# Kernel optimization log

Measured on AMD Instinct MI355X. Metric: run time of the kernel, lower is better.

## Reference

```python
import jax, jax.numpy as jnp
import numpy as np

S, B, V, E, H = 64, 32, 32000, 512, 1024


def gru_cell(x, h, Wih, Whh, bih, bhh):
    # PyTorch GRU cell math. x: [B, in], h: [B, H]
    gi = x @ Wih.T + bih          # [B, 3H]
    gh = h @ Whh.T + bhh          # [B, 3H]
    ir, iz, inn = jnp.split(gi, 3, axis=-1)
    hr, hz, hn = jnp.split(gh, 3, axis=-1)
    r = jax.nn.sigmoid(ir + hr)
    z = jax.nn.sigmoid(iz + hz)
    n = jnp.tanh(inn + r * hn)
    return (1.0 - z) * n + z * h


def run_gru(xs, h0, Wih, Whh, bih, bhh):
    def step(h, x):
        h = gru_cell(x, h, Wih, Whh, bih, bhh)
        return h, h
    _, hs = jax.lax.scan(step, h0, xs)
    return hs  # [S, B, H]


def setup_inputs():
    key = jax.random.key(0)
    ks = jax.random.split(key, 24)
    n = lambda k, shp, s=0.05: (jax.random.normal(k, shp, jnp.float32) * s)
    inp = {
        "input_seq": jax.random.randint(ks[0], (S, B), 0, V),
        "target_seq": jax.random.randint(ks[1], (S, B), 0, V),
        "emb": n(ks[2], (V, E)),
        # bidirectional encoder GRU (forward / backward directions)
        "enc_Wih_f": n(ks[3], (3 * H, E)), "enc_Whh_f": n(ks[4], (3 * H, H)),
        "enc_bih_f": n(ks[5], (3 * H,)),  "enc_bhh_f": n(ks[6], (3 * H,)),
        "enc_Wih_b": n(ks[7], (3 * H, E)), "enc_Whh_b": n(ks[8], (3 * H, H)),
        "enc_bih_b": n(ks[9], (3 * H,)),  "enc_bhh_b": n(ks[10], (3 * H,)),
        "encoder_init": n(ks[11], (2, H), 0.1),
        # decoder GRU: input = token(E) + glimpse(2H) + last_output(E)
        "dec_Wih": n(ks[12], (3 * H, 2 * E + 2 * H)), "dec_Whh": n(ks[13], (3 * H, H)),
        "dec_bih": n(ks[14], (3 * H,)), "dec_bhh": n(ks[15], (3 * H,)),
        "dec_init_h": n(ks[16], (H,), 0.1),
        "dec_init_out": n(ks[17], (E,), 0.1),
        "attn_W1": n(ks[18], (H, 3 * H)),  # Linear(3H -> H, bias=False)
        "attn_W2": n(ks[19], (1, H)),      # Linear(H -> 1, bias=False)
        "out_W": n(ks[20], (V, H)), "out_b": n(ks[21], (V,)),
    }
    return inp


def reference(input_seq, target_seq, emb,
              enc_Wih_f, enc_Whh_f, enc_bih_f, enc_bhh_f,
              enc_Wih_b, enc_Whh_b, enc_bih_b, enc_bhh_b, encoder_init,
              dec_Wih, dec_Whh, dec_bih, dec_bhh, dec_init_h, dec_init_out,
              attn_W1, attn_W2, out_W, out_b):
    x = emb[input_seq]            # [S, B, E]
    tgt = emb[target_seq]         # [S, B, E]
    bsz = x.shape[1]

    # bidirectional encoder
    h0f = jnp.broadcast_to(encoder_init[0], (bsz, H))
    h0b = jnp.broadcast_to(encoder_init[1], (bsz, H))
    fwd = run_gru(x, h0f, enc_Wih_f, enc_Whh_f, enc_bih_f, enc_bhh_f)
    bwd = run_gru(x[::-1], h0b, enc_Wih_b, enc_Whh_b, enc_bih_b, enc_bhh_b)[::-1]
    enc = jnp.concatenate([fwd, bwd], axis=-1)  # [S, B, 2H]

    def step(carry, inp_t):
        h, last_out = carry                      # [B,H], [B,E]
        tok, tg = inp_t                          # [B,E], [B,E]
        hexp = jnp.broadcast_to(h[None], (S, bsz, H))
        a = jnp.concatenate([enc, hexp], axis=-1)            # [S, B, 3H]
        scores = jnp.tanh(a @ attn_W1.T) @ attn_W2.T          # [S, B, 1]
        # NOTE: original uses nn.Softmax(dim=1) on [S,B,1] -> softmax over BATCH dim
        w = jax.nn.softmax(scores, axis=1)
        glimpse = (enc * w).sum(axis=0)                       # [B, 2H]
        dec_in = jnp.concatenate([tok, glimpse, last_out], axis=-1)
        h = gru_cell(dec_in, h, dec_Wih, dec_Whh, dec_bih, dec_bhh)
        probs = jax.nn.softmax(h @ out_W.T + out_b, axis=1)   # [B, V]
        return (h, tg), probs

    h0 = jnp.broadcast_to(dec_init_h, (bsz, H))
    o0 = jnp.broadcast_to(dec_init_out, (bsz, E))
    _, outs = jax.lax.scan(step, (h0, o0), (x, tgt))
    return outs  # [S, B, V]
```

## Files before the change

### kernel.cpp

```cpp
#include <hip/hip_runtime.h>
#include <hip/hip_bf16.h>

#define S_ 64
#define B_ 32
#define V_ 32000
#define E_ 512
#define H_ 1024
#define H3_ 3072

typedef __hip_bfloat16 bf16;
typedef __attribute__((ext_vector_type(8))) short s8v;
typedef __attribute__((ext_vector_type(4))) float f4;
typedef unsigned long long ull;

__device__ __forceinline__ float b2f(bf16 x){ return __bfloat162float(x); }
__device__ __forceinline__ bf16  f2b(float x){ return __float2bfloat16(x); }
__device__ __forceinline__ float bfu2f(unsigned short u){
  union { unsigned u; float f; } c; c.u = ((unsigned)u) << 16; return c.f;
}
#define MFMA16(a,b,c) __builtin_amdgcn_mfma_f32_16x16x32_bf16((a),(b),(c),0,0,0)

__device__ __forceinline__ float fsigmoid(float x){ return 1.f/(1.f + __expf(-x)); }
__device__ __forceinline__ float ftanh(float x){ float e2 = __expf(2.f*x); return 1.f - 2.f/(e2 + 1.f); }

__global__ __launch_bounds__(256) void cast_bf16_k(const float* __restrict__ s, bf16* __restrict__ d, int n8){
  int stride = gridDim.x*256;
  for (int i = blockIdx.x*256 + threadIdx.x; i < n8; i += stride){
    f4 a = *((const f4*)s + (size_t)i*2);
    f4 b = *((const f4*)s + (size_t)i*2 + 1);
    union { s8v v; bf16 h[8]; } o;
    #pragma unroll
    for (int k=0;k<4;k++){ o.h[k]=f2b(a[k]); o.h[4+k]=f2b(b[k]); }
    *((s8v*)d + i) = o.v;
  }
}
__global__ __launch_bounds__(256) void cast2_k(const float* __restrict__ s0, const float* __restrict__ s1,
                                               bf16* __restrict__ d0, bf16* __restrict__ d1, int n8){
  const float* s = blockIdx.y ? s1 : s0;
  bf16* d = blockIdx.y ? d1 : d0;
  int stride = gridDim.x*256;
  for (int i = blockIdx.x*256 + threadIdx.x; i < n8; i += stride){
    f4 a = *((const f4*)s + (size_t)i*2);
    f4 b = *((const f4*)s + (size_t)i*2 + 1);
    union { s8v v; bf16 h[8]; } o;
    #pragma unroll
    for (int k=0;k<4;k++){ o.h[k]=f2b(a[k]); o.h[4+k]=f2b(b[k]); }
    *((s8v*)d + i) = o.v;
  }
}
__global__ __launch_bounds__(256) void cast4_k(const float* __restrict__ s0, const float* __restrict__ s1,
                                               const float* __restrict__ s2, const float* __restrict__ s3,
                                               bf16* __restrict__ d0, bf16* __restrict__ d1,
                                               bf16* __restrict__ d2, bf16* __restrict__ d3, int n8){
  const float* s = (blockIdx.y==0)?s0:(blockIdx.y==1)?s1:(blockIdx.y==2)?s2:s3;
  bf16* d = (blockIdx.y==0)?d0:(blockIdx.y==1)?d1:(blockIdx.y==2)?d2:d3;
  int stride = gridDim.x*256;
  for (int i = blockIdx.x*256 + threadIdx.x; i < n8; i += stride){
    f4 a = *((const f4*)s + (size_t)i*2);
    f4 b = *((const f4*)s + (size_t)i*2 + 1);
    union { s8v v; bf16 h[8]; } o;
    #pragma unroll
    for (int k=0;k<4;k++){ o.h[k]=f2b(a[k]); o.h[4+k]=f2b(b[k]); }
    *((s8v*)d + i) = o.v;
  }
}
__global__ __launch_bounds__(256) void gather2_k(const float* __restrict__ emb,
                                                 const int* __restrict__ iseq, const int* __restrict__ tseq,
                                                 const float* __restrict__ o0,
                                                 bf16* __restrict__ dx, bf16* __restrict__ dlo){
  int i = blockIdx.x*256 + threadIdx.x;
  int row = i >> 6, e8 = i & 63;
  const float* src;
  bf16* d;
  if (blockIdx.y == 0){
    src = emb + (size_t)iseq[row]*E_;
    d = dx;
  } else {
    int t = row >> 5, b = row & 31;
    src = (t == 0) ? o0 : (emb + (size_t)tseq[(t-1)*B_ + b]*E_);
    d = dlo;
  }
  f4 a = *((const f4*)src + e8*2);
  f4 b = *((const f4*)src + e8*2 + 1);
  union { s8v v; bf16 h[8]; } o;
  #pragma unroll
  for (int k=0;k<4;k++){ o.h[k]=f2b(a[k]); o.h[4+k]=f2b(b[k]); }
  *((s8v*)d + i) = o.v;
}

template<int WB16, int ACC>
__global__ __launch_bounds__(256) void gemm_bt(const bf16* __restrict__ A, int lda,
                                               const bf16* __restrict__ B, int ldb,
                                               const float* __restrict__ bias,
                                               void* __restrict__ Cp, int ldc, int K)
{
  __shared__ bf16 a_sm[128][40];
  __shared__ bf16 b_sm[128][40];
  const int tid = threadIdx.x;
  const int m0 = blockIdx.y*128, n0 = blockIdx.x*128;
  const int w = tid>>6, l = tid&63;
  const int wm = w>>1, wn = w&1;
  f4 acc[4][4];
  #pragma unroll
  for (int i=0;i<4;i++)
    #pragma unroll
    for (int j=0;j<4;j++) acc[i][j] = (f4){0.f,0.f,0.f,0.f};
  const int srow = tid>>1, skc = (tid&1)*16;
  const int ar = l&15, koff = (l>>4)*8;
  for (int k0 = 0; k0 < K; k0 += 32){
    __syncthreads();
    const s8v* pa = (const s8v*)(A + (size_t)(m0+srow)*lda + k0 + skc);
    const s8v* pb = (const s8v*)(B + (size_t)(n0+srow)*ldb + k0 + skc);
    *(s8v*)&a_sm[srow][skc]   = pa[0];
    *(s8v*)&a_sm[srow][skc+8] = pa[1];
    *(s8v*)&b_sm[srow][skc]   = pb[0];
    *(s8v*)&b_sm[srow][skc+8] = pb[1];
    __syncthreads();
    s8v av[4], bv[4];
    #pragma unroll
    for (int i=0;i<4;i++) av[i] = *(const s8v*)&a_sm[wm*64 + i*16 + ar][koff];
    #pragma unroll
    for (int j=0;j<4;j++) bv[j] = *(const s8v*)&b_sm[wn*64 + j*16 + ar][koff];
    #pragma unroll
    for (int i=0;i<4;i++)
      #pragma unroll
      for (int j=0;j<4;j++)
        acc[i][j] = MFMA16(av[i], bv[j], acc[i][j]);
  }
  const int rb = (l>>4)*4;
  #pragma unroll
  for (int i=0;i<4;i++){
    #pragma unroll
    for (int j=0;j<4;j++){
      int col = n0 + wn*64 + j*16 + ar;
      float badd = bias ? bias[col] : 0.f;
      #pragma unroll
      for (int r=0;r<4;r++){
        int row = m0 + wm*64 + i*16 + rb + r;
        size_t idx = (size_t)row*ldc + col;
        float v = acc[i][j][r] + badd;
        if (ACC) v += ((const float*)Cp)[idx];
        if (WB16) ((bf16*)Cp)[idx] = f2b(v);
        else      ((float*)Cp)[idx] = v;
      }
    }
  }
}

__global__ __launch_bounds__(256) void out_gemm_k(
  const bf16* __restrict__ A, const bf16* __restrict__ Bw,
  const float* __restrict__ bias, bf16* __restrict__ C)
{
  __shared__ bf16 a_sm[128][40];
  __shared__ bf16 b_sm[128][40];
  const int tid = threadIdx.x;
  const int bid = blockIdx.x;
  const int xcd = bid & 7, kk = bid >> 3;
  const int super = kk >> 6, rem = kk & 63;
  const int sm = super & 1, sn = super >> 1;
  const int mi = rem & 7, nj = rem >> 3;
  const int mt = sm*8 + mi, nl = sn*8 + nj;
  const int nt = nl*8 + xcd;
  if (nt >= 250) return;
  const int m0 = mt*128, n0 = nt*128;
  const int w = tid>>6, l = tid&63;
  const int wm = w>>1, wn = w&1;
  f4 acc[4][4];
  #pragma unroll
  for (int i=0;i<4;i++)
    #pragma unroll
    for (int j=0;j<4;j++) acc[i][j] = (f4){0.f,0.f,0.f,0.f};
  const int srow = tid>>1, skc = (tid&1)*16;
  const int ar = l&15, koff = (l>>4)*8;
  for (int k0 = 0; k0 < 1024; k0 += 32){
    __syncthreads();
    const s8v* pa = (const s8v*)(A + (size_t)(m0+srow)*1024 + k0 + skc);
    const s8v* pb = (const s8v*)(Bw + (size_t)(n0+srow)*1024 + k0 + skc);
    *(s8v*)&a_sm[srow][skc]   = pa[0];
    *(s8v*)&a_sm[srow][skc+8] = pa[1];
    *(s8v*)&b_sm[srow][skc]   = pb[0];
    *(s8v*)&b_sm[srow][skc+8] = pb[1];
    __syncthreads();
    s8v av[4], bv[4];
    #pragma unroll
    for (int i=0;i<4;i++) av[i] = *(const s8v*)&a_sm[wm*64 + i*16 + ar][koff];
    #pragma unroll
    for (int j=0;j<4;j++) bv[j] = *(const s8v*)&b_sm[wn*64 + j*16 + ar][koff];
    #pragma unroll
    for (int i=0;i<4;i++)
      #pragma unroll
      for (int j=0;j<4;j++)
        acc[i][j] = MFMA16(av[i], bv[j], acc[i][j]);
  }
  const int rb = (l>>4)*4;
  float bj[4];
  #pragma unroll
  for (int j=0;j<4;j++) bj[j] = bias[n0 + wn*64 + j*16 + ar];
  #pragma unroll
  for (int i=0;i<4;i++){
    #pragma unroll
    for (int j=0;j<4;j++){
      const int col = n0 + wn*64 + j*16 + ar;
      #pragma unroll
      for (int r=0;r<4;r++){
        const int row = m0 + wm*64 + i*16 + rb + r;
        C[(size_t)row*V_ + col] = f2b(acc[i][j][r] + bj[j]);
      }
    }
  }
}

__global__ __launch_bounds__(256) void logit_stats_k(const bf16* __restrict__ lg,
                                                     float* __restrict__ rowM, float* __restrict__ rowL){
  __shared__ float wm[4], wl[4];
  const int tid = threadIdx.x;
  const bf16* p = lg + (size_t)blockIdx.x*V_;
  float m = -1e30f, lsum = 0.f;
  for (int c = tid; c < V_/8; c += 256){
    union { s8v v; unsigned short us[8]; } u;
    u.v = *((const s8v*)p + c);
    #pragma unroll
    for (int k = 0; k < 8; ++k){
      float v = bfu2f(u.us[k]);
      float mn = fmaxf(m, v);
      lsum = lsum*__expf(m - mn) + __expf(v - mn);
      m = mn;
    }
  }
  #pragma unroll
  for (int o = 32; o; o >>= 1){
    float mo = __shfl_xor(m, o), lo_ = __shfl_xor(lsum, o);
    float mn = fmaxf(m, mo);
    lsum = lsum*__expf(m - mn) + lo_*__expf(mo - mn);
    m = mn;
  }
  if ((tid&63)==0){ wm[tid>>6] = m; wl[tid>>6] = lsum; }
  __syncthreads();
  if (tid == 0){
    float M = fmaxf(fmaxf(wm[0],wm[1]), fmaxf(wm[2],wm[3]));
    float L = wl[0]*__expf(wm[0]-M) + wl[1]*__expf(wm[1]-M)
            + wl[2]*__expf(wm[2]-M) + wl[3]*__expf(wm[3]-M);
    rowM[blockIdx.x] = M;
    rowL[blockIdx.x] = L;
  }
}

__global__ __launch_bounds__(256) void norm_k(const bf16* __restrict__ lg,
                                              const float* __restrict__ rowM, const float* __restrict__ rowL,
                                              float* __restrict__ out){
  const int tid = threadIdx.x;
  const int row = blockIdx.x;
  const float M = rowM[row], inv = 1.f/rowL[row];
  const bf16* p = lg + (size_t)row*V_;
  float* q = out + (size_t)row*V_;
  for (int c = tid; c < V_/8; c += 256){
    union { s8v v; unsigned short us[8]; } u;
    u.v = *((const s8v*)p + c);
    f4 o0, o1;
    #pragma unroll
    for (int k = 0; k < 4; ++k) o0[k] = __expf(bfu2f(u.us[k]) - M)*inv;
    #pragma unroll
    for (int k = 0; k < 4; ++k) o1[k] = __expf(bfu2f(u.us[4+k]) - M)*inv;
    *((f4*)q + c*2)     = o0;
    *((f4*)q + c*2 + 1) = o1;
  }
}

__global__ __launch_bounds__(256) void enc_init_k(const float* __restrict__ enc_init,
                                                  const float* __restrict__ bihf, const float* __restrict__ bihb,
                                                  bf16* __restrict__ hb0, float* __restrict__ hfE,
                                                  float* __restrict__ bias_fb){
  int i = blockIdx.x*256 + threadIdx.x;
  int base = i*8;
  int dir = base>>15, rem = base&32767, col = rem&1023;
  const float* sp = enc_init + dir*H_ + col;
  f4 a = *(const f4*)sp, b = *(const f4*)(sp+4);
  union { s8v v; bf16 h[8]; } o;
  #pragma unroll
  for (int k=0;k<4;k++){ o.h[k]=f2b(a[k]); o.h[4+k]=f2b(b[k]); }
  *(s8v*)(hb0 + dir*32768 + rem) = o.v;
  *(f4*)(hfE + dir*32768 + rem) = a;
  *(f4*)(hfE + dir*32768 + rem + 4) = b;
  if (i < 6144) bias_fb[i] = (i < 3072) ? bihf[i] : bihb[i-3072];
}
__global__ __launch_bounds__(256) void dec_init_k(const float* __restrict__ dinh,
                                                  bf16* __restrict__ hd0, float* __restrict__ hfD){
  int i = blockIdx.x*256 + threadIdx.x;
  int base = i*8;
  int col = base&1023;
  const float* sp = dinh + col;
  f4 a = *(const f4*)sp, b = *(const f4*)(sp+4);
  union { s8v v; bf16 h[8]; } o;
  #pragma unroll
  for (int k=0;k<4;k++){ o.h[k]=f2b(a[k]); o.h[4+k]=f2b(b[k]); }
  *(s8v*)(hd0 + base) = o.v;
  *(f4*)(hfD + base) = a;
  *(f4*)(hfD + base + 4) = b;
}

__global__ __launch_bounds__(256) void enc_step_k(
  const float* __restrict__ gi_fb,
  const bf16* __restrict__ whhf, const bf16* __restrict__ whhb,
  const float* __restrict__ bhhf, const float* __restrict__ bhhb,
  const bf16* __restrict__ hrd_base, bf16* __restrict__ hwr_base,
  float* __restrict__ hfE, bf16* __restrict__ enc_out, int s)
{
  __shared__ bf16 hst[16][1032];
  __shared__ bf16 hsT[16][64];
  const int tid = threadIdx.x, bid = blockIdx.x;
  const int w = tid>>6, l = tid&63;
  const int lr = l&15, koff = (l>>4)*8, rb = (l>>4)*4;
  const int x = bid&7, g3 = bid>>3;
  const int dir = x>>2;
  const int mt = g3>>2;
  const int jtb = (x&3)*16 + (g3&3)*4;
  const int jt = jtb + w;
  const int col = jt*16 + lr;
  const bf16* W    = dir ? whhb : whhf;
  const float* bhh = dir ? bhhb : bhhf;
  const float br_ = bhh[col], bz_ = bhh[H_+col], bn_ = bhh[2*H_+col];
  const bf16* pr = W + (size_t)(jt*16 + lr)*H_ + koff;
  const bf16* pz = pr + (size_t)H_*H_;
  const bf16* pn = pz + (size_t)H_*H_;
  {
    const bf16* src = hrd_base + dir*32768 + (size_t)mt*16*H_;
    #pragma unroll
    for (int c = 0; c < 8; ++c){
      int g = c*256 + tid;
      int row = g>>7, off = g&127;
      *(s8v*)&hst[row][off*8] = *(const s8v*)(src + (size_t)row*H_ + off*8);
    }
  }
  __syncthreads();
  f4 accr = (f4){0,0,0,0}, accz = (f4){0,0,0,0}, accn = (f4){0,0,0,0};
  #pragma unroll 4
  for (int k0 = 0; k0 < H_; k0 += 32){
    s8v a = *(const s8v*)&hst[lr][koff + k0];
    accr = MFMA16(a, *(const s8v*)(pr + k0), accr);
    accz = MFMA16(a, *(const s8v*)(pz + k0), accz);
    accn = MFMA16(a, *(const s8v*)(pn + k0), accn);
  }
  const int es = dir ? (63 - s) : s;
  const int dcol = dir*3072 + col;
  #pragma unroll
  for (int ri = 0; ri < 4; ++ri){
    const int b_ = mt*16 + rb + ri;
    const size_t gr = (size_t)(es*B_ + b_)*6144;
    float ir = gi_fb[gr + dcol], iz = gi_fb[gr + 1024 + dcol], inn = gi_fb[gr + 2048 + dcol];
    float rg = fsigmoid(ir + accr[ri] + br_);
    float zg = fsigmoid(iz + accz[ri] + bz_);
    float ng = ftanh(inn + rg*(accn[ri] + bn_));
    float hold = hfE[dir*32768 + b_*H_ + col];
    float hnew = (1.f - zg)*ng + zg*hold;
    hfE[dir*32768 + b_*H_ + col] = hnew;
    hsT[rb+ri][w*16+lr] = f2b(hnew);
  }
  __syncthreads();
  {
    const int row = tid>>4, seg = tid&15;
    ull v = *(ull*)&hsT[row][seg*4];
    *(ull*)(hwr_base + dir*32768 + (size_t)(mt*16+row)*H_ + jtb*16 + seg*4) = v;
    *(ull*)(enc_out + (size_t)(es*B_ + mt*16+row)*2048 + dir*H_ + jtb*16 + seg*4) = v;
  }
}

__global__ __launch_bounds__(256) void dec_k1(
  const bf16* __restrict__ hd,
  const bf16* __restrict__ whhd, const float* __restrict__ bhhd,
  const bf16* __restrict__ w1b,
  float* __restrict__ gh, bf16* __restrict__ hW1b)
{
  __shared__ bf16 hst[16][1032];
  __shared__ float ghT[16][128];
  __shared__ bf16 hwT[16][128];
  const int tid = threadIdx.x, bid = blockIdx.x;
  const int w = tid>>6, l = tid&63;
  const int lr = l&15, koff = (l>>4)*8;
  const bool isP = bid < 16;
  const int hmt = isP ? (bid&1) : ((bid-16)&1);
  {
    const bf16* src = hd + (size_t)hmt*16*H_;
    #pragma unroll
    for (int c = 0; c < 8; ++c){
      int g = c*256 + tid;
      int row = g>>7, off = g&127;
      *(s8v*)&hst[row][off*8] = *(const s8v*)(src + (size_t)row*H_ + off*8);
    }
  }
  __syncthreads();
  if (isP){
    const int x2 = bid>>1;
    const int pjt0 = x2*8 + w*2;
    #pragma unroll
    for (int q = 0; q < 2; ++q){
      const bf16* pb = w1b + (size_t)((pjt0+q)*16 + lr)*H3_ + 2048 + koff;
      f4 acc = (f4){0,0,0,0};
      #pragma unroll 4
      for (int k0 = 0; k0 < H_; k0 += 32)
        acc = MFMA16(*(const s8v*)&hst[lr][koff+k0], *(const s8v*)(pb+k0), acc);
      #pragma unroll
      for (int r = 0; r < 4; ++r)
        hwT[(l>>4)*4+r][(w*2+q)*16 + lr] = f2b(acc[r]);
    }
    __syncthreads();
    #pragma unroll
    for (int i = 0; i < 2; ++i){
      int idx = tid + i*256;
      int row = idx>>5, seg = idx&31;
      *(ull*)(hW1b + (size_t)(hmt*16+row)*H_ + x2*128 + seg*4) = *(ull*)&hwT[row][seg*4];
    }
  } else {
    const int gb = bid - 16;
    const int rest = gb>>1;
    const int x3 = rest/3, gkk = rest%3;
    const int ntb = x3*24 + gkk*8;
    #pragma unroll
    for (int q = 0; q < 2; ++q){
      const int nt = ntb + w*2 + q;
      const bf16* pb = whhd + (size_t)(nt*16 + lr)*H_ + koff;
      const float bv = bhhd[nt*16 + lr];
      f4 acc = (f4){0,0,0,0};
      #pragma unroll 4
      for (int k0 = 0; k0 < H_; k0 += 32)
        acc = MFMA16(*(const s8v*)&hst[lr][koff+k0], *(const s8v*)(pb+k0), acc);
      #pragma unroll
      for (int r = 0; r < 4; ++r)
        ghT[(l>>4)*4+r][(w*2+q)*16 + lr] = acc[r] + bv;
    }
    __syncthreads();
    #pragma unroll
    for (int i = 0; i < 4; ++i){
      int idx = tid + i*256;
      int row = idx>>6, seg = idx&63;
      union{ float f[2]; ull u; } pk;
      pk.f[0] = ghT[row][seg*2]; pk.f[1] = ghT[row][seg*2+1];
      *(ull*)(gh + (size_t)(hmt*16+row)*H3_ + ntb*16 + seg*2) = pk.u;
    }
  }
}

__global__ __launch_bounds__(256) void dec_k2(
  const bf16* __restrict__ encW1b, const bf16* __restrict__ hW1b,
  const float* __restrict__ attnW2, float* __restrict__ wat)
{
  __shared__ float w2st[1024];
  __shared__ float scl[32];
  const int tid = threadIdx.x, s = blockIdx.x;
  w2st[tid] = attnW2[tid];
  w2st[tid+256] = attnW2[tid+256];
  w2st[tid+512] = attnW2[tid+512];
  w2st[tid+768] = attnW2[tid+768];
  __syncthreads();
  const int b = tid>>3, part = tid&7;
  const bf16* hp = hW1b + (size_t)b*H_ + part*128;
  const bf16* ep = encW1b + ((size_t)s*B_ + b)*H_ + part*128;
  const float* wp = w2st + part*128;
  float p = 0.f;
  #pragma unroll 4
  for (int ii = 0; ii < 16; ++ii){
    union { s8v v; unsigned short uu[8]; } hv, ev;
    hv.v = *(const s8v*)(hp + ii*8);
    ev.v = *(const s8v*)(ep + ii*8);
    #pragma unroll
    for (int k = 0; k < 8; ++k){
      float xx = bfu2f(ev.uu[k]) + bfu2f(hv.uu[k]);
      p += wp[ii*8+k]*ftanh(xx);
    }
  }
  p += __shfl_xor(p,1); p += __shfl_xor(p,2); p += __shfl_xor(p,4);
  if (part == 0) scl[b] = p;
  __syncthreads();
  if (tid < 32){
    float v = scl[tid];
    float m = v;
    #pragma unroll
    for (int o = 1; o <= 16; o <<= 1) m = fmaxf(m, __shfl_xor(m, o));
    float e = __expf(v - m);
    float Z = e;
    #pragma unroll
    for (int o = 1; o <= 16; o <<= 1) Z += __shfl_xor(Z, o);
    wat[s*B_ + tid] = e/Z;
  }
}

__global__ __launch_bounds__(256) void dec_k3(
  const float* __restrict__ gi_t,
  const bf16* __restrict__ encWgb, const float* __restrict__ gh,
  const float* __restrict__ wat,
  float* __restrict__ hfD, bf16* __restrict__ hd_w, bf16* __restrict__ hall_t)
{
  __shared__ float watst[64];
  __shared__ float part_[4][3][256];
  __shared__ bf16 hnewst[256];
  const int tid = threadIdx.x, bid = blockIdx.x;
  const int x = bid&7, g3 = bid>>3;
  const int db = 4*x + (g3&3), jq = g3>>2;
  const int jD = jq*256 + tid;
  if (tid < 64) watst[tid] = wat[tid*B_ + db];
  __syncthreads();
  const int lane = tid&63, wv = tid>>6;
  const int j0 = jq*256 + lane*4;
  f4 g0 = (f4){0,0,0,0}, g1 = (f4){0,0,0,0}, g2 = (f4){0,0,0,0};
  #pragma unroll 4
  for (int i = 0; i < 16; ++i){
    const int s2 = wv*16 + i;
    const float wt = watst[s2];
    const bf16* ro = encWgb + ((size_t)s2*B_ + db)*H3_;
    union{ ull u; unsigned short us[4]; } v0, v1, v2;
    v0.u = *(const ull*)(ro + j0);
    v1.u = *(const ull*)(ro + H_ + j0);
    v2.u = *(const ull*)(ro + 2*H_ + j0);
    #pragma unroll
    for (int k = 0; k < 4; ++k){
      g0[k] += wt*bfu2f(v0.us[k]);
      g1[k] += wt*bfu2f(v1.us[k]);
      g2[k] += wt*bfu2f(v2.us[k]);
    }
  }
  *(f4*)&part_[wv][0][lane*4] = g0;
  *(f4*)&part_[wv][1][lane*4] = g1;
  *(f4*)&part_[wv][2][lane*4] = g2;
  __syncthreads();
  float G0 = part_[0][0][tid]+part_[1][0][tid]+part_[2][0][tid]+part_[3][0][tid];
  float G1 = part_[0][1][tid]+part_[1][1][tid]+part_[2][1][tid]+part_[3][1][tid];
  float G2 = part_[0][2][tid]+part_[1][2][tid]+part_[2][2][tid]+part_[3][2][tid];
  const float* gp = gi_t + (size_t)db*H3_ + jD;
  float ir  = gp[0]    + G0;
  float iz  = gp[H_]   + G1;
  float inn = gp[2*H_] + G2;
  float hr_ = gh[(size_t)db*H3_ + jD];
  float hz_ = gh[(size_t)db*H3_ + H_ + jD];
  float hn_ = gh[(size_t)db*H3_ + 2*H_ + jD];
  float rg = fsigmoid(ir + hr_);
  float zg = fsigmoid(iz + hz_);
  float ng = ftanh(inn + rg*hn_);
  float hold = hfD[(size_t)db*H_ + jD];
  float hnew = (1.f - zg)*ng + zg*hold;
  hfD[(size_t)db*H_ + jD] = hnew;
  hnewst[tid] = f2b(hnew);
  __syncthreads();
  if (tid < 64){
    ull v = *(ull*)&hnewst[tid*4];
    *(ull*)(hd_w + (size_t)db*H_ + jq*256 + tid*4) = v;
    *(ull*)(hall_t + (size_t)db*H_ + jq*256 + tid*4) = v;
  }
}

extern "C" void kernel_launch(void* const* d_in, const int* in_sizes, int n_in,
                              void* d_out, int out_size, void* d_ws, size_t ws_size,
                              hipStream_t stream)
{
  (void)in_sizes; (void)n_in; (void)out_size; (void)ws_size;
  const int*   iseq  = (const int*)d_in[0];
  const int*   tseq  = (const int*)d_in[1];
  const float* emb   = (const float*)d_in[2];
  const float* wihf  = (const float*)d_in[3];
  const float* whhf_f= (const float*)d_in[4];
  const float* bihf  = (const float*)d_in[5];
  const float* bhhf  = (const float*)d_in[6];
  const float* wihb  = (const float*)d_in[7];
  const float* whhb_f= (const float*)d_in[8];
  const float* bihb  = (const float*)d_in[9];
  const float* bhhb  = (const float*)d_in[10];
  const float* einit = (const float*)d_in[11];
  const float* wihd  = (const float*)d_in[12];
  const float* whhd_f= (const float*)d_in[13];
  const float* bihd  = (const float*)d_in[14];
  const float* bhhd  = (const float*)d_in[15];
  const float* dinh  = (const float*)d_in[16];
  const float* dino  = (const float*)d_in[17];
  const float* w1    = (const float*)d_in[18];
  const float* w2    = (const float*)d_in[19];
  const float* outw  = (const float*)d_in[20];
  const float* outb  = (const float*)d_in[21];
  float* out = (float*)d_out;

  char* ws = (char*)d_ws;
  size_t off = 0;
  auto alloc = [&](size_t bytes)->char*{ char* p = ws + off; off += (bytes + 255) & ~(size_t)255; return p; };
  bf16* logits_b = (bf16*)ws;
  bf16* x_b      = (bf16*)alloc((size_t)2048*512*2);
  bf16* lo_b     = (bf16*)alloc((size_t)2048*512*2);
  bf16* wihf_b   = (bf16*)alloc((size_t)3072*512*2);
  bf16* wihb_b   = (bf16*)alloc((size_t)3072*512*2);
  bf16* whhf_b   = (bf16*)alloc((size_t)3072*1024*2);
  bf16* whhb_b   = (bf16*)alloc((size_t)3072*1024*2);
  bf16* wihd_b   = (bf16*)alloc((size_t)3072*3072*2);
  bf16* whhd_b   = (bf16*)alloc((size_t)3072*1024*2);
  bf16* w1_b     = (bf16*)alloc((size_t)1024*3072*2);
  float* gi_fb   = (float*)alloc((size_t)2048*6144*4);
  float* gi_d    = (float*)alloc((size_t)2048*3072*4);
  bf16* enc_b    = (bf16*)alloc((size_t)2048*2048*2);
  bf16* encW1_b  = (bf16*)alloc((size_t)2048*1024*2);
  bf16* encWg_b  = (bf16*)alloc((size_t)2048*3072*2);
  float* bias_fb = (float*)alloc((size_t)6144*4);
  bf16*  henc_b  = (bf16*)alloc((size_t)2*65536*2);
  float* hfE     = (float*)alloc((size_t)2*32768*4);
  bf16*  hdb     = (bf16*)alloc((size_t)2*32768*2);
  float* hfD     = (float*)alloc((size_t)32768*4);
  bf16*  hW1b    = (bf16*)alloc((size_t)32768*2);
  float* ghb     = (float*)alloc((size_t)32*3072*4);
  float* wat     = (float*)alloc((size_t)64*32*4);
  float* rowM    = (float*)alloc((size_t)2048*4);
  float* rowL    = (float*)alloc((size_t)2048*4);
  bf16* outw_b   = (bf16*)alloc((size_t)32000*1024*2);
  bf16*  hall_b  = (bf16*)alloc((size_t)2048*1024*2);

  gather2_k<<<dim3(512,2), 256, 0, stream>>>(emb, iseq, tseq, dino, x_b, lo_b);
  cast2_k<<<dim3(768,2),  256, 0, stream>>>(wihf, wihb, wihf_b, wihb_b, 196608);
  cast4_k<<<dim3(768,4),  256, 0, stream>>>(whhf_f, whhb_f, whhd_f, w1,
                                            whhf_b, whhb_b, whhd_b, w1_b, 393216);
  cast_bf16_k<<<2048, 256, 0, stream>>>(wihd, wihd_b, 1179648);
  cast_bf16_k<<<2048, 256, 0, stream>>>(outw, outw_b, 4096000);
  enc_init_k<<<32, 256, 0, stream>>>(einit, bihf, bihb, henc_b, hfE, bias_fb);

  gemm_bt<0,0><<<dim3(48,16), 256, 0, stream>>>(x_b, 512, wihf_b,      512,  bias_fb, gi_fb, 6144, 512);
  gemm_bt<0,0><<<dim3(24,16), 256, 0, stream>>>(x_b, 512, wihd_b,      3072, bihd,    gi_d,  3072, 512);
  gemm_bt<0,1><<<dim3(24,16), 256, 0, stream>>>(lo_b,512, wihd_b+2560, 3072, nullptr, gi_d,  3072, 512);

  for (int s = 0; s < 64; ++s){
    const bf16* hrd = henc_b + (size_t)(s&1)*65536;
    bf16*       hwr = henc_b + (size_t)((s+1)&1)*65536;
    enc_step_k<<<64, 256, 0, stream>>>(gi_fb, whhf_b, whhb_b, bhhf, bhhb,
                                       hrd, hwr, hfE, enc_b, s);
  }

  gemm_bt<1,0><<<dim3(8,16),  256, 0, stream>>>(enc_b, 2048, w1_b,       3072, nullptr, encW1_b, 1024, 2048);
  gemm_bt<1,0><<<dim3(24,16), 256, 0, stream>>>(enc_b, 2048, wihd_b+512, 3072, nullptr, encWg_b, 3072, 2048);

  dec_init_k<<<16, 256, 0, stream>>>(dinh, hdb, hfD);
  for (int t = 0; t < 64; ++t){
    const bf16* hdr = hdb + (size_t)(t&1)*32768;
    bf16*       hdw = hdb + (size_t)((t+1)&1)*32768;
    dec_k1<<<64, 256, 0, stream>>>(hdr, whhd_b, bhhd, w1_b, ghb, hW1b);
    dec_k2<<<64, 256, 0, stream>>>(encW1_b, hW1b, w2, wat);
    dec_k3<<<128, 256, 0, stream>>>(gi_d + (size_t)t*B_*H3_, encWg_b, ghb, wat,
                                    hfD, hdw, hall_b + (size_t)t*B_*H_);
  }

  out_gemm_k<<<4096, 256, 0, stream>>>(hall_b, outw_b, outb, logits_b);
  logit_stats_k<<<2048, 256, 0, stream>>>(logits_b, rowM, rowL);
  norm_k<<<2048, 256, 0, stream>>>(logits_b, rowM, rowL, out);
}
```

Baseline: 3.162 ms.

## Fuse attention score computation into decoder h-projection kernel, drop separate score kernel

The attention-score kernel is removed from the per-step decoder loop. Each projection block of the first kernel now computes partial tanh-score sums over its 128-column slice of W1 for all 64 positions and writes them to an 8-way partial buffer. The GRU-update kernel sums those partials and does the batch softmax itself. This removes one launch and the bf16 round trip of h·W1 per step. In exchange, the 16 projection blocks do much more serial work, and every GRU block redundantly reduces all partials and recomputes the softmax.

New measurement: 4.302 ms. +36.0%, slower.

```diff
diff --git a/kernel.cpp b/kernel.cpp
--- a/kernel.cpp
+++ b/kernel.cpp
@@ -364,20 +364,26 @@
   }
 }
 
-__global__ __launch_bounds__(256) void dec_k1(
+__global__ __launch_bounds__(256) void dec_kA(
   const bf16* __restrict__ hd,
   const bf16* __restrict__ whhd, const float* __restrict__ bhhd,
   const bf16* __restrict__ w1b,
-  float* __restrict__ gh, bf16* __restrict__ hW1b)
+  const bf16* __restrict__ encW1b,
+  const float* __restrict__ attnW2,
+  float* __restrict__ gh,
+  float* __restrict__ sc8)
 {
   __shared__ bf16 hst[16][1032];
   __shared__ float ghT[16][128];
-  __shared__ bf16 hwT[16][128];
+  __shared__ float hwf2[4][16][33];
+  __shared__ float scp[64][17];
+  __shared__ float w2s2[4][33];
   const int tid = threadIdx.x, bid = blockIdx.x;
   const int w = tid>>6, l = tid&63;
   const int lr = l&15, koff = (l>>4)*8;
   const bool isP = bid < 16;
   const int hmt = isP ? (bid&1) : ((bid-16)&1);
+  const int x2 = bid>>1;
   {
     const bf16* src = hd + (size_t)hmt*16*H_;
     #pragma unroll
@@ -387,9 +393,9 @@
       *(s8v*)&hst[row][off*8] = *(const s8v*)(src + (size_t)row*H_ + off*8);
     }
   }
+  if (isP && tid < 128) w2s2[tid>>5][tid&31] = attnW2[x2*128 + tid];
   __syncthreads();
   if (isP){
-    const int x2 = bid>>1;
     const int pjt0 = x2*8 + w*2;
     #pragma unroll
     for (int q = 0; q < 2; ++q){
@@ -398,16 +404,39 @@
       #pragma unroll 4
       for (int k0 = 0; k0 < H_; k0 += 32)
         acc = MFMA16(*(const s8v*)&hst[lr][koff+k0], *(const s8v*)(pb+k0), acc);
+      const int jl = (w*2+q);
       #pragma unroll
       for (int r = 0; r < 4; ++r)
-        hwT[(l>>4)*4+r][(w*2+q)*16 + lr] = f2b(acc[r]);
+        hwf2[jl>>1][(l>>4)*4+r][(jl&1)*16 + lr] = acc[r];
     }
     __syncthreads();
-    #pragma unroll
-    for (int i = 0; i < 2; ++i){
-      int idx = tid + i*256;
-      int row = idx>>5, seg = idx&31;
-      *(ull*)(hW1b + (size_t)(hmt*16+row)*H_ + x2*128 + seg*4) = *(ull*)&hwT[row][seg*4];
+    const int bl = l&15, jg = l>>4;
+    const bf16* ebase = encW1b + ((size_t)(hmt*16 + bl))*H_ + x2*128 + jg*32;
+    for (int si = 0; si < 16; ++si){
+      const int s = w*16 + si;
+      const bf16* ep = ebase + (size_t)s*B_*H_;
+      float pp = 0.f;
+      #pragma unroll
+      for (int c8 = 0; c8 < 4; ++c8){
+        union{ s8v v; unsigned short us[8]; } ev;
+        ev.v = *(const s8v*)(ep + c8*8);
+        #pragma unroll
+        for (int k = 0; k < 8; ++k){
+          const int jj = c8*8 + k;
+          pp += w2s2[jg][jj]*ftanh(bfu2f(ev.us[k]) + hwf2[jg][bl][jj]);
+        }
+      }
+      pp += __shfl_xor(pp, 16);
+      pp += __shfl_xor(pp, 32);
+      if (l < 16) scp[s][l] = pp;
+    }
+    __syncthreads();
+    {
+      const int s = tid>>2, v4 = tid&3;
+      f4 o;
+      o[0] = scp[s][v4*4];   o[1] = scp[s][v4*4+1];
+      o[2] = scp[s][v4*4+2]; o[3] = scp[s][v4*4+3];
+      *(f4*)(sc8 + (size_t)x2*2048 + s*32 + hmt*16 + v4*4) = o;
     }
   } else {
     const int gb = bid - 16;
@@ -439,56 +468,13 @@
   }
 }
 
-__global__ __launch_bounds__(256) void dec_k2(
-  const bf16* __restrict__ encW1b, const bf16* __restrict__ hW1b,
-  const float* __restrict__ attnW2, float* __restrict__ wat)
-{
-  __shared__ float w2st[1024];
-  __shared__ float scl[32];
-  const int tid = threadIdx.x, s = blockIdx.x;
-  w2st[tid] = attnW2[tid];
-  w2st[tid+256] = attnW2[tid+256];
-  w2st[tid+512] = attnW2[tid+512];
-  w2st[tid+768] = attnW2[tid+768];
-  __syncthreads();
-  const int b = tid>>3, part = tid&7;
-  const bf16* hp = hW1b + (size_t)b*H_ + part*128;
-  const bf16* ep = encW1b + ((size_t)s*B_ + b)*H_ + part*128;
-  const float* wp = w2st + part*128;
-  float p = 0.f;
-  #pragma unroll 4
-  for (int ii = 0; ii < 16; ++ii){
-    union { s8v v; unsigned short uu[8]; } hv, ev;
-    hv.v = *(const s8v*)(hp + ii*8);
-    ev.v = *(const s8v*)(ep + ii*8);
-    #pragma unroll
-    for (int k = 0; k < 8; ++k){
-      float xx = bfu2f(ev.uu[k]) + bfu2f(hv.uu[k]);
-      p += wp[ii*8+k]*ftanh(xx);
-    }
-  }
-  p += __shfl_xor(p,1); p += __shfl_xor(p,2); p += __shfl_xor(p,4);
-  if (part == 0) scl[b] = p;
-  __syncthreads();
-  if (tid < 32){
-    float v = scl[tid];
-    float m = v;
-    #pragma unroll
-    for (int o = 1; o <= 16; o <<= 1) m = fmaxf(m, __shfl_xor(m, o));
-    float e = __expf(v - m);
-    float Z = e;
-    #pragma unroll
-    for (int o = 1; o <= 16; o <<= 1) Z += __shfl_xor(Z, o);
-    wat[s*B_ + tid] = e/Z;
-  }
-}
-
-__global__ __launch_bounds__(256) void dec_k3(
+__global__ __launch_bounds__(256) void dec_kB(
   const float* __restrict__ gi_t,
   const bf16* __restrict__ encWgb, const float* __restrict__ gh,
-  const float* __restrict__ wat,
+  const float* __restrict__ sc8,
   float* __restrict__ hfD, bf16* __restrict__ hd_w, bf16* __restrict__ hall_t)
 {
+  __shared__ float scc2[64][33];
   __shared__ float watst[64];
   __shared__ float part_[4][3][256];
   __shared__ bf16 hnewst[256];
@@ -496,7 +482,28 @@
   const int x = bid&7, g3 = bid>>3;
   const int db = 4*x + (g3&3), jq = g3>>2;
   const int jD = jq*256 + tid;
-  if (tid < 64) watst[tid] = wat[tid*B_ + db];
+  {
+    const int base = tid*8, s = base>>5, b0 = base&31;
+    f4 a0 = (f4){0,0,0,0}, a1 = (f4){0,0,0,0};
+    #pragma unroll
+    for (int x2 = 0; x2 < 8; ++x2){
+      a0 += *(const f4*)(sc8 + (size_t)x2*2048 + base);
+      a1 += *(const f4*)(sc8 + (size_t)x2*2048 + base + 4);
+    }
+    #pragma unroll
+    for (int k = 0; k < 4; ++k){ scc2[s][b0+k] = a0[k]; scc2[s][b0+4+k] = a1[k]; }
+  }
+  __syncthreads();
+  if (tid < 64){
+    const int s = tid;
+    float m = -1e30f;
+    #pragma unroll 8
+    for (int b = 0; b < 32; ++b) m = fmaxf(m, scc2[s][b]);
+    float Z = 0.f;
+    #pragma unroll 8
+    for (int b = 0; b < 32; ++b) Z += __expf(scc2[s][b] - m);
+    watst[s] = __expf(scc2[s][db] - m)/Z;
+  }
   __syncthreads();
   const int lane = tid&63, wv = tid>>6;
   const int j0 = jq*256 + lane*4;
@@ -598,9 +605,8 @@
   float* hfE     = (float*)alloc((size_t)2*32768*4);
   bf16*  hdb     = (bf16*)alloc((size_t)2*32768*2);
   float* hfD     = (float*)alloc((size_t)32768*4);
-  bf16*  hW1b    = (bf16*)alloc((size_t)32768*2);
   float* ghb     = (float*)alloc((size_t)32*3072*4);
-  float* wat     = (float*)alloc((size_t)64*32*4);
+  float* sc8     = (float*)alloc((size_t)8*64*32*4);
   float* rowM    = (float*)alloc((size_t)2048*4);
   float* rowL    = (float*)alloc((size_t)2048*4);
   bf16* outw_b   = (bf16*)alloc((size_t)32000*1024*2);
@@ -632,9 +638,8 @@
   for (int t = 0; t < 64; ++t){
     const bf16* hdr = hdb + (size_t)(t&1)*32768;
     bf16*       hdw = hdb + (size_t)((t+1)&1)*32768;
-    dec_k1<<<64, 256, 0, stream>>>(hdr, whhd_b, bhhd, w1_b, ghb, hW1b);
-    dec_k2<<<64, 256, 0, stream>>>(encW1_b, hW1b, w2, wat);
-    dec_k3<<<128, 256, 0, stream>>>(gi_d + (size_t)t*B_*H3_, encWg_b, ghb, wat,
+    dec_kA<<<64, 256, 0, stream>>>(hdr, whhd_b, bhhd, w1_b, encW1_b, w2, ghb, sc8);
+    dec_kB<<<128, 256, 0, stream>>>(gi_d + (size_t)t*B_*H3_, encWg_b, ghb, sc8,
                                     hfD, hdw, hall_b + (size_t)t*B_*H_);
   }
 
```
